# Kernel optimization log

Measured on AMD Instinct MI355X. Metric: run time of the kernel, lower is better.

The kernel has to match this reference:

```python
import jax, jax.numpy as jnp
import numpy as np

S = 1024   # speakers_per_batch
U = 64     # utterances_per_speaker
E = 256    # model_embedding_size


def setup_inputs() -> dict:
    key = jax.random.key(0)
    k1, _ = jax.random.split(key)
    # embeds as produced by forward(): relu'd then L2-normalized rows
    raw = jax.nn.relu(jax.random.normal(k1, (S * U, E), dtype=jnp.float32))
    embeds = raw / (jnp.linalg.norm(raw, axis=1, keepdims=True) + 1e-12)
    return {
        "embeds": embeds,
        "similarity_weight": jnp.array([10.0], dtype=jnp.float32),
        "similarity_bias": jnp.array([-5.0], dtype=jnp.float32),
    }


def reference(embeds, similarity_weight, similarity_bias):
    e = embeds.reshape(S, U, E)                      # [S,U,E]
    # inclusive centroids (per speaker)
    c_incl = jnp.mean(e, axis=1)                     # [S,E]
    incl_norm = jnp.linalg.norm(c_incl, axis=1)      # [S]
    # exclusive centroids (leave-one-out per utterance)
    c_excl = (jnp.sum(e, axis=1, keepdims=True) - e) / (U - 1)  # [S,U,E]
    excl_norm = jnp.linalg.norm(c_excl, axis=2)      # [S,U]
    # off-diagonal (k != j): cosine vs inclusive centroid of speaker k
    sim = jnp.einsum('jue,ke->juk', e, c_incl) / incl_norm       # [S,U,S]
    # diagonal (k == j): cosine vs own exclusive centroid
    diag = jnp.einsum('jue,jue->ju', e, c_excl) / excl_norm      # [S,U]
    idx = jnp.arange(S)
    sim = sim.at[idx, :, idx].set(diag)
    sim = sim * similarity_weight[0] + similarity_bias[0]
    # cross-entropy against ground truth speaker ids
    logits = sim.reshape(S * U, S)                   # [SU,S]
    gt = jnp.repeat(jnp.arange(S), U)                # [SU]
    logp = jax.nn.log_softmax(logits, axis=-1)
    loss = -jnp.mean(jnp.take_along_axis(logp, gt[:, None], axis=1))
    preds = jnp.argmax(logits, axis=1)
    accuracy = jnp.mean((preds == gt).astype(jnp.float32))
    return loss, accuracy
```

## Files before the change

### kernel.cpp

```cpp
#include <hip/hip_runtime.h>
#include <math.h>

#define NS 1024
#define NU 64
#define NE 256

typedef __attribute__((ext_vector_type(4))) float f32x4;
typedef __attribute__((ext_vector_type(16))) float f32x16;
typedef long i64x2 __attribute__((ext_vector_type(2)));

__device__ static inline unsigned int pk4_fp8(float a, float b, float c,
                                              float d) {
  int r = 0;
  r = __builtin_amdgcn_cvt_pk_fp8_f32(a, b, r, false);
  r = __builtin_amdgcn_cvt_pk_fp8_f32(c, d, r, true);
  return (unsigned int)r;
}


__global__ __launch_bounds__(256) void centroid_kernel(
    const float* __restrict__ embeds, unsigned int* __restrict__ Cb,
    unsigned long long* __restrict__ Ab, float* __restrict__ normsum,
    float* __restrict__ ssumG, unsigned int* __restrict__ pmaxG,
    float* __restrict__ out) {
  int k = blockIdx.x;
  int t = threadIdx.x;
  if (t < 64) {
    ssumG[k * 64 + t] = 0.f;
    pmaxG[k * 64 + t] = 0u;
  }
  int wave = t >> 6, e4 = t & 63;

  const float4* base =
      (const float4*)(embeds + (size_t)k * NU * NE) + wave * 16 * 64 + e4;
  float4 s = {0.f, 0.f, 0.f, 0.f};
#pragma unroll
  for (int i = 0; i < 16; ++i) {
    float4 v = base[i * 64];
    s.x += v.x; s.y += v.y; s.z += v.z; s.w += v.w;
  }
  __shared__ float4 ps[4][64];
  ps[wave][e4] = s;
  __syncthreads();
  if (t < 64) {
    float4 a = ps[0][t], b = ps[1][t], c = ps[2][t], d = ps[3][t];
    float4 s4;
    s4.x = a.x + b.x + c.x + d.x;
    s4.y = a.y + b.y + c.y + d.y;
    s4.z = a.z + b.z + c.z + d.z;
    s4.w = a.w + b.w + c.w + d.w;
    float sq = s4.x * s4.x + s4.y * s4.y + s4.z * s4.z + s4.w * s4.w;
#pragma unroll
    for (int off = 32; off; off >>= 1) sq += __shfl_xor(sq, off, 64);
    float nrm = sqrtf(sq);
    float inv = 1.f / nrm;
    unsigned int v = pk4_fp8(s4.x * inv, s4.y * inv, s4.z * inv, s4.w * inv);
    int lane_ = (k & 31) + 32 * ((t >> 1) & 1);
    int idx = (k >> 5) * 2048 + (t >> 3) * 256 + lane_ * 4 +
              (((t >> 2) & 1) << 1) + (t & 1);
    Cb[idx] = v;
    if (t == 0) {
      normsum[k] = nrm;
      if (k == 0) { out[0] = 0.f; out[1] = 0.f; }
    }
  }

  {
    int tt = t >> 7;
    int l = t & 63;
    int hp = (t >> 6) & 1;
    int row = k * 64 + tt * 32 + (l & 31);
    int kbase = (l >> 5) * 8;
    const float* rowp = embeds + (size_t)row * NE;
    i64x2* Ab2 = (i64x2*)Ab;
    size_t rt = (size_t)k * 2 + tt;
#pragma unroll
    for (int i = 0; i < 4; ++i) {
      int sp = hp * 4 + i;
      unsigned long long u[2];
#pragma unroll
      for (int half = 0; half < 2; ++half) {
        int sI = 2 * sp + half;
        int k0 = sI * 16 + kbase;
        float4 x = *(const float4*)(rowp + k0);
        float4 y = *(const float4*)(rowp + k0 + 4);
        unsigned int lo = pk4_fp8(x.x, x.y, x.z, x.w);
        unsigned int hi = pk4_fp8(y.x, y.y, y.z, y.w);
        u[half] = ((unsigned long long)hi << 32) | lo;
      }
      i64x2 v;
      v.x = (long)u[0];
      v.y = (long)u[1];
      Ab2[(rt * 8 + sp) * 64 + l] = v;
    }
  }
}

__global__ __launch_bounds__(256) void main_kernel(
    const long* __restrict__ Ab, const long* __restrict__ Cb,
    const float* __restrict__ normsum, const float* __restrict__ wp,
    const float* __restrict__ bp, float* __restrict__ ssumG,
    unsigned int* __restrict__ pmaxG, float* __restrict__ pdiagG) {
  int t = threadIdx.x;
  int wave = t >> 6, lane = t & 63;
  int hi = lane >> 5;
  int b = blockIdx.x;
  int rg = b >> 1;
  int h = b & 1;
  int jspk = rg * 2 + (wave >> 1);
  int r0 = rg * 128 + wave * 32;

  float w = *wp, bia = *bp;
  const float L2E = 1.4426950408889634f;
  float M0 = fabsf(w) + bia;
  float wl = w * L2E;
  float cl = (bia - M0) * L2E;
  float ns = normsum[jspk];

  const i64x2* Av = (const i64x2*)Ab;
  const i64x2* Bv = (const i64x2*)Cb;
  int gt_base = h * 16;

  long af[16];
  {
    int rt = rg * 4 + wave;
#pragma unroll
    for (int sp = 0; sp < 8; ++sp) {
      i64x2 v = Av[(rt * 8 + sp) * 64 + lane];
      af[2 * sp] = v.x;
      af[2 * sp + 1] = v.y;
    }
  }

  float ssum[16], pm[16];
#pragma unroll
  for (int i = 0; i < 16; ++i) {
    ssum[i] = 0.f;
    pm[i] = 0.f;
  }

  auto loadBA = [&](i64x2 (&BF)[4], int ct) {
    int cb = (gt_base + ct) * 512 + lane;
#pragma unroll
    for (int sp = 0; sp < 4; ++sp) BF[sp] = Bv[cb + sp * 64];
  };
  auto loadBB = [&](i64x2 (&BF)[4], int ct) {
    int cb = (gt_base + ct) * 512 + lane + 256;
#pragma unroll
    for (int i = 0; i < 4; ++i) BF[i] = Bv[cb + i * 64];
  };

  auto tile = [&](f32x16& ACC, i64x2 (&BA)[4], i64x2 (&BB)[4], int nextT) {
    f32x16 a;
#pragma unroll
    for (int i = 0; i < 16; ++i) a[i] = 0.f;
    int nt = nextT < 16 ? nextT : 15;
#pragma unroll
    for (int sp = 0; sp < 4; ++sp) {
      a = __builtin_amdgcn_mfma_f32_32x32x16_fp8_fp8(af[2 * sp], BA[sp].x, a,
                                                     0, 0, 0);
      a = __builtin_amdgcn_mfma_f32_32x32x16_fp8_fp8(af[2 * sp + 1], BA[sp].y,
                                                     a, 0, 0, 0);
    }
    loadBA(BA, nt);
#pragma unroll
    for (int sp = 0; sp < 4; ++sp) {
      a = __builtin_amdgcn_mfma_f32_32x32x16_fp8_fp8(af[8 + 2 * sp], BB[sp].x,
                                                     a, 0, 0, 0);
      a = __builtin_amdgcn_mfma_f32_32x32x16_fp8_fp8(af[9 + 2 * sp], BB[sp].y,
                                                     a, 0, 0, 0);
    }
    loadBB(BB, nt);
    ACC = a;
  };

  auto epilogue = [&](f32x16& ACC, int T) {
    int gt = gt_base + T;
    bool diagstep = ((jspk >> 5) == gt);
    f32x16 a = ACC;
    if (diagstep && (lane & 31) == (jspk & 31)) {
#pragma unroll
      for (int i = 0; i < 16; ++i) {
        float Sv = a[i] * ns;
        float den = fmaxf(fmaf(ns, ns, 1.f) - 2.f * Sv, 1e-30f);
        float val = (Sv - 1.f) * __frsqrt_rn(den);
        float pd = __builtin_amdgcn_exp2f(fmaf(val, wl, cl));
        pdiagG[r0 + (i & 3) + 8 * (i >> 2) + 4 * hi] = pd;
        a[i] = val;
      }
    }
#pragma unroll
    for (int i = 0; i < 16; ++i) {
      float p = __builtin_amdgcn_exp2f(fmaf(a[i], wl, cl));
      ssum[i] += p;
      pm[i] = fmaxf(pm[i], p);
    }
  };

  i64x2 BA[4], BB[4];
  f32x16 accA, accB;
  loadBA(BA, 0);
  loadBB(BB, 0);
  tile(accA, BA, BB, 1);
#pragma unroll 1
  for (int T = 1; T < 15; T += 2) {
    tile(accB, BA, BB, T + 1);
    epilogue(accA, T - 1);
    tile(accA, BA, BB, T + 2);
    epilogue(accB, T);
  }
  tile(accB, BA, BB, 16);
  epilogue(accA, 14);
  epilogue(accB, 15);

#pragma unroll
  for (int i = 0; i < 16; ++i) {
    float s = ssum[i];
    s += __shfl_xor(s, 1, 64);
    s += __shfl_xor(s, 2, 64);
    s += __shfl_xor(s, 4, 64);
    s += __shfl_xor(s, 8, 64);
    s += __shfl_xor(s, 16, 64);
    float m = pm[i];
    m = fmaxf(m, __shfl_xor(m, 1, 64));
    m = fmaxf(m, __shfl_xor(m, 2, 64));
    m = fmaxf(m, __shfl_xor(m, 4, 64));
    m = fmaxf(m, __shfl_xor(m, 8, 64));
    m = fmaxf(m, __shfl_xor(m, 16, 64));
    if ((lane & 31) == 0) {
      int row = r0 + (i & 3) + 8 * (i >> 2) + 4 * hi;
      atomicAdd(&ssumG[row], s);
      atomicMax(&pmaxG[row], __float_as_uint(m));
    }
  }
}

__global__ __launch_bounds__(256) void reduce_kernel(
    const float* __restrict__ ssumG, const unsigned int* __restrict__ pmaxG,
    const float* __restrict__ pdiagG, float* __restrict__ out) {
  int i = blockIdx.x * 256 + threadIdx.x;
  float pd = pdiagG[i];
  float lossr = __logf(ssumG[i] / pd);
  float corr = (pd >= __uint_as_float(pmaxG[i])) ? 1.f : 0.f;
#pragma unroll
  for (int off = 32; off; off >>= 1) {
    lossr += __shfl_xor(lossr, off, 64);
    corr += __shfl_xor(corr, off, 64);
  }
  __shared__ float pl[4], pc[4];
  int wave = threadIdx.x >> 6, lane = threadIdx.x & 63;
  if (lane == 0) { pl[wave] = lossr; pc[wave] = corr; }
  __syncthreads();
  if (threadIdx.x == 0) {
    const float inv = 1.f / (float)(NS * NU);
    atomicAdd(&out[0], (pl[0] + pl[1] + pl[2] + pl[3]) * inv);
    atomicAdd(&out[1], (pc[0] + pc[1] + pc[2] + pc[3]) * inv);
  }
}

extern "C" void kernel_launch(void* const* d_in, const int* in_sizes, int n_in,
                              void* d_out, int out_size, void* d_ws,
                              size_t ws_size, hipStream_t stream) {
  const float* embeds = (const float*)d_in[0];
  const float* w = (const float*)d_in[1];
  const float* b = (const float*)d_in[2];
  float* out = (float*)d_out;
  char* ws = (char*)d_ws;
  unsigned int* Cb = (unsigned int*)ws;
  unsigned int* pmaxG = (unsigned int*)(ws + (256 << 10));
  float* ssumG = (float*)(ws + (512 << 10));
  float* pdiagG = (float*)(ws + (768 << 10));
  float* normsum = (float*)(ws + (1024 << 10));
  unsigned long long* Ab =
      (unsigned long long*)(ws + (1056 << 10));

  centroid_kernel<<<NS, 256, 0, stream>>>(embeds, Cb, Ab, normsum, ssumG,
                                          pmaxG, out);
  main_kernel<<<1024, 256, 0, stream>>>((const long*)Ab, (const long*)Cb,
                                        normsum, w, b, ssumG, pmaxG, pdiagG);
  reduce_kernel<<<NS * NU / 256, 256, 0, stream>>>(ssumG, pmaxG, pdiagG, out);
}
```

Baseline: 151.9 us.

## Fuse fp8 A-operand conversion into main kernel and stagger centroid tile order

The centroid kernel no longer converts every embedding row to a pre-packed fp8 buffer. The main kernel now reads the fp32 rows directly and packs them to fp8 in registers. This removes a write and re-read of the intermediate A buffer, but each main block now reads four times as many A bytes. In addition, each block starts its 16 centroid tiles at a rotated offset derived from the block id, to spread concurrent blocks across different B tiles and cut contention on the same cache lines.

Measured after the change: 149.7 us. No clear change (-1.4%).

```diff
diff --git a/kernel.cpp b/kernel.cpp
--- a/kernel.cpp
+++ b/kernel.cpp
@@ -20,9 +20,8 @@
 
 __global__ __launch_bounds__(256) void centroid_kernel(
     const float* __restrict__ embeds, unsigned int* __restrict__ Cb,
-    unsigned long long* __restrict__ Ab, float* __restrict__ normsum,
-    float* __restrict__ ssumG, unsigned int* __restrict__ pmaxG,
-    float* __restrict__ out) {
+    float* __restrict__ normsum, float* __restrict__ ssumG,
+    unsigned int* __restrict__ pmaxG, float* __restrict__ out) {
   int k = blockIdx.x;
   int t = threadIdx.x;
   if (t < 64) {
@@ -64,40 +63,10 @@
       if (k == 0) { out[0] = 0.f; out[1] = 0.f; }
     }
   }
-
-  {
-    int tt = t >> 7;
-    int l = t & 63;
-    int hp = (t >> 6) & 1;
-    int row = k * 64 + tt * 32 + (l & 31);
-    int kbase = (l >> 5) * 8;
-    const float* rowp = embeds + (size_t)row * NE;
-    i64x2* Ab2 = (i64x2*)Ab;
-    size_t rt = (size_t)k * 2 + tt;
-#pragma unroll
-    for (int i = 0; i < 4; ++i) {
-      int sp = hp * 4 + i;
-      unsigned long long u[2];
-#pragma unroll
-      for (int half = 0; half < 2; ++half) {
-        int sI = 2 * sp + half;
-        int k0 = sI * 16 + kbase;
-        float4 x = *(const float4*)(rowp + k0);
-        float4 y = *(const float4*)(rowp + k0 + 4);
-        unsigned int lo = pk4_fp8(x.x, x.y, x.z, x.w);
-        unsigned int hi = pk4_fp8(y.x, y.y, y.z, y.w);
-        u[half] = ((unsigned long long)hi << 32) | lo;
-      }
-      i64x2 v;
-      v.x = (long)u[0];
-      v.y = (long)u[1];
-      Ab2[(rt * 8 + sp) * 64 + l] = v;
-    }
-  }
 }
 
 __global__ __launch_bounds__(256) void main_kernel(
-    const long* __restrict__ Ab, const long* __restrict__ Cb,
+    const float* __restrict__ embeds, const long* __restrict__ Cb,
     const float* __restrict__ normsum, const float* __restrict__ wp,
     const float* __restrict__ bp, float* __restrict__ ssumG,
     unsigned int* __restrict__ pmaxG, float* __restrict__ pdiagG) {
@@ -117,18 +86,20 @@
   float cl = (bia - M0) * L2E;
   float ns = normsum[jspk];
 
-  const i64x2* Av = (const i64x2*)Ab;
   const i64x2* Bv = (const i64x2*)Cb;
   int gt_base = h * 16;
+  int start = (b * 5) & 15;
 
   long af[16];
   {
-    int rt = rg * 4 + wave;
-#pragma unroll
-    for (int sp = 0; sp < 8; ++sp) {
-      i64x2 v = Av[(rt * 8 + sp) * 64 + lane];
-      af[2 * sp] = v.x;
-      af[2 * sp + 1] = v.y;
+    const float* rowp = embeds + (size_t)(r0 + (lane & 31)) * NE + hi * 8;
+#pragma unroll
+    for (int s = 0; s < 16; ++s) {
+      float4 x = *(const float4*)(rowp + s * 16);
+      float4 y = *(const float4*)(rowp + s * 16 + 4);
+      unsigned int lo = pk4_fp8(x.x, x.y, x.z, x.w);
+      unsigned int hh = pk4_fp8(y.x, y.y, y.z, y.w);
+      af[s] = (long)(((unsigned long long)hh << 32) | lo);
     }
   }
 
@@ -150,11 +121,10 @@
     for (int i = 0; i < 4; ++i) BF[i] = Bv[cb + i * 64];
   };
 
-  auto tile = [&](f32x16& ACC, i64x2 (&BA)[4], i64x2 (&BB)[4], int nextT) {
+  auto tile = [&](f32x16& ACC, i64x2 (&BA)[4], i64x2 (&BB)[4], int nextCt) {
     f32x16 a;
 #pragma unroll
     for (int i = 0; i < 16; ++i) a[i] = 0.f;
-    int nt = nextT < 16 ? nextT : 15;
 #pragma unroll
     for (int sp = 0; sp < 4; ++sp) {
       a = __builtin_amdgcn_mfma_f32_32x32x16_fp8_fp8(af[2 * sp], BA[sp].x, a,
@@ -162,7 +132,7 @@
       a = __builtin_amdgcn_mfma_f32_32x32x16_fp8_fp8(af[2 * sp + 1], BA[sp].y,
                                                      a, 0, 0, 0);
     }
-    loadBA(BA, nt);
+    loadBA(BA, nextCt);
 #pragma unroll
     for (int sp = 0; sp < 4; ++sp) {
       a = __builtin_amdgcn_mfma_f32_32x32x16_fp8_fp8(af[8 + 2 * sp], BB[sp].x,
@@ -170,12 +140,12 @@
       a = __builtin_amdgcn_mfma_f32_32x32x16_fp8_fp8(af[9 + 2 * sp], BB[sp].y,
                                                      a, 0, 0, 0);
     }
-    loadBB(BB, nt);
+    loadBB(BB, nextCt);
     ACC = a;
   };
 
-  auto epilogue = [&](f32x16& ACC, int T) {
-    int gt = gt_base + T;
+  auto epilogue = [&](f32x16& ACC, int ct) {
+    int gt = gt_base + ct;
     bool diagstep = ((jspk >> 5) == gt);
     f32x16 a = ACC;
     if (diagstep && (lane & 31) == (jspk & 31)) {
@@ -197,21 +167,22 @@
     }
   };
 
+  auto ct = [&](int i) { return (start + i) & 15; };
   i64x2 BA[4], BB[4];
   f32x16 accA, accB;
-  loadBA(BA, 0);
-  loadBB(BB, 0);
-  tile(accA, BA, BB, 1);
+  loadBA(BA, ct(0));
+  loadBB(BB, ct(0));
+  tile(accA, BA, BB, ct(1));
 #pragma unroll 1
   for (int T = 1; T < 15; T += 2) {
-    tile(accB, BA, BB, T + 1);
-    epilogue(accA, T - 1);
-    tile(accA, BA, BB, T + 2);
-    epilogue(accB, T);
-  }
-  tile(accB, BA, BB, 16);
-  epilogue(accA, 14);
-  epilogue(accB, 15);
+    tile(accB, BA, BB, ct(T + 1));
+    epilogue(accA, ct(T - 1));
+    tile(accA, BA, BB, ct(T + 2 < 16 ? T + 2 : 15));
+    epilogue(accB, ct(T));
+  }
+  tile(accB, BA, BB, ct(15));
+  epilogue(accA, ct(14));
+  epilogue(accB, ct(15));
 
 #pragma unroll
   for (int i = 0; i < 16; ++i) {
@@ -271,12 +242,10 @@
   float* ssumG = (float*)(ws + (512 << 10));
   float* pdiagG = (float*)(ws + (768 << 10));
   float* normsum = (float*)(ws + (1024 << 10));
-  unsigned long long* Ab =
-      (unsigned long long*)(ws + (1056 << 10));
-
-  centroid_kernel<<<NS, 256, 0, stream>>>(embeds, Cb, Ab, normsum, ssumG,
-                                          pmaxG, out);
-  main_kernel<<<1024, 256, 0, stream>>>((const long*)Ab, (const long*)Cb,
-                                        normsum, w, b, ssumG, pmaxG, pdiagG);
+
+  centroid_kernel<<<NS, 256, 0, stream>>>(embeds, Cb, normsum, ssumG, pmaxG,
+                                          out);
+  main_kernel<<<1024, 256, 0, stream>>>(embeds, (const long*)Cb, normsum, w, b,
+                                        ssumG, pmaxG, pdiagG);
   reduce_kernel<<<NS * NU / 256, 256, 0, stream>>>(ssumG, pmaxG, pdiagG, out);
 }
```
